# Performance work log

Measured on AMD Instinct MI355X. Metric: run time of the kernel, lower is better.

## Reference

```python
import jax, jax.numpy as jnp
import numpy as np

B, C, T = 2048, 8, 1024
EPS = 1e-5
SLOPE = 1.0 / 128.0


def leaky(x):
    # F.leaky_relu(x, 1/128)
    return jnp.where(x >= 0, x, SLOPE * x)


def batchnorm(h, g, b):
    # training-mode BatchNorm1d over [B, C, T]: stats over (batch, time), biased var
    m = h.mean(axis=(0, 2), keepdims=True)
    v = jnp.mean((h - m) ** 2, axis=(0, 2), keepdims=True)
    return (h - m) * jax.lax.rsqrt(v + EPS) * g[None, :, None] + b[None, :, None]


def setup_inputs() -> dict:
    key = jax.random.key(0)
    ks = jax.random.split(key, 8)
    x = jax.random.normal(ks[0], (B, C, T), dtype=jnp.float32)
    # reservoir pushforward: low-bit random matrix scaled to spectral radius 0.1
    A_raw = jax.random.normal(ks[1], (C, C), dtype=jnp.float32)
    rho = jnp.max(jnp.abs(np.linalg.eigvals(np.asarray(A_raw))))
    A = (0.1 * A_raw / rho).astype(jnp.float32)
    w1 = jax.random.normal(ks[2], (24, 8), dtype=jnp.float32) * (1.0 / np.sqrt(8))
    b1 = jax.random.normal(ks[3], (24,), dtype=jnp.float32) * 0.01
    w2 = jax.random.normal(ks[4], (16, 24), dtype=jnp.float32) * (1.0 / np.sqrt(24))
    b2 = jax.random.normal(ks[5], (16,), dtype=jnp.float32) * 0.01
    w3 = jax.random.normal(ks[6], (11, 48), dtype=jnp.float32) * (1.0 / np.sqrt(48))
    b3 = jax.random.normal(ks[7], (11,), dtype=jnp.float32) * 0.01
    return {
        "x": x, "A": A,
        "bn1_g": jnp.ones((8,), jnp.float32), "bn1_b": jnp.zeros((8,), jnp.float32),
        "w1": w1, "b1": b1, "w2": w2, "b2": b2, "w3": w3, "b3": b3,
        "bn2_g": jnp.ones((11,), jnp.float32), "bn2_b": jnp.zeros((11,), jnp.float32),
    }


def reference(x, A, bn1_g, bn1_b, w1, b1, w2, b2, w3, b3, bn2_g, bn2_b):
    bw = batchnorm(x, bn1_g, bn1_b)  # [B,8,T]

    # --- FSDDRC reservoir: 1024-step sequential recurrence on 8-dim state ---
    xs = jnp.transpose(bw, (2, 0, 1))  # [T,B,8]

    def step(f, xt):
        # nonlin(A @ f + x_t) with nonlin(z) = clamp(4z, -1, 1)
        f_new = jnp.clip(4.0 * (f @ A.T + xt), -1.0, 1.0)
        return f_new, jnp.concatenate([f_new, leaky(f_new)], axis=-1)  # [B,16]

    f0 = jnp.zeros_like(xs[0])
    _, outs = jax.lax.scan(step, f0, xs)  # [T,B,16]
    nl_tdyn = jnp.transpose(outs, (1, 2, 0))  # [B,16,T]

    # --- feedforward branch (mtmt = linear over channel dim) ---
    h = leaky(jnp.einsum("bct,oc->bot", bw, w1) + b1[None, :, None])  # [B,24,T]
    ff = leaky(jnp.einsum("bct,oc->bot", h, w2) + b2[None, :, None])  # [B,16,T]

    stacked = jnp.concatenate([x, bw, ff, nl_tdyn], axis=1)  # [B,48,T]
    pre = jnp.einsum("bct,oc->bot", stacked, w3) + b3[None, :, None]  # [B,11,T]
    assimilated = leaky(batchnorm(pre, bn2_g, bn2_b))
    return assimilated.mean(axis=-1)  # [B,11]
```

## Files before the change

### kernel.cpp

```cpp
#include <hip/hip_runtime.h>
#include <hip/hip_fp16.h>

#define NB 2048
#define NC 8
#define NT 1024
#define EPS 1e-5f
#define SLOPE (1.0f/128.0f)
#define NELEM (2048.0f*1024.0f)
#define TB (NT*NB)

#define PAR_OFF 9216
#define BN2_OFF 1024
#define PF_S4  0
#define PF_O4  8
#define PF_B1F 16
#define PF_B2F 40
#define PF_B3F 56
#define PU_A4   96
#define PU_W1   128
#define PU_W2   224
#define PU_W3X  416
#define PU_W3F  460
#define PU_W3L  504
#define PU_W3FF 548
#define XT_BYTE  65536
#define PWS_BYTE (65536 + 2048*1024*8*2)

typedef _Float16 h2 __attribute__((ext_vector_type(2)));
typedef __fp16  fp16v2 __attribute__((ext_vector_type(2)));
union U32H2 { unsigned u; h2 h; fp16v2 f; unsigned short us[2]; };

__device__ __forceinline__ float leaky(float z){ return fmaxf(z, z*SLOPE); }
__device__ __forceinline__ unsigned short f2h(float v){ return __half_as_ushort(__float2half(v)); }
__device__ __forceinline__ float h2f(unsigned short u){ return __half2float(__ushort_as_half(u)); }
__device__ __forceinline__ h2 uph2(unsigned u){ U32H2 x; x.u = u; return x.h; }
__device__ __forceinline__ h2 pk(float a, float b){
    U32H2 x; x.f = __builtin_amdgcn_cvt_pkrtz(a, b); return x.h;
}
__device__ __forceinline__ h2 leaky2(h2 v){
    h2 s = v * (_Float16)SLOPE;
    return __builtin_elementwise_max(v, s);
}
__device__ __forceinline__ float clamp1(float z){ return __builtin_amdgcn_fmed3f(z, -1.f, 1.f); }

#if defined(__has_builtin)
#if __has_builtin(__builtin_amdgcn_fdot2)
#define HAVE_FDOT2 1
#endif
#endif
#ifdef HAVE_FDOT2
__device__ __forceinline__ float fdot2(h2 a, h2 b, float c){ return __builtin_amdgcn_fdot2(a, b, c, false); }
#else
__device__ __forceinline__ float fdot2(h2 a, h2 b, float c){
    return c + (float)a[0]*(float)b[0] + (float)a[1]*(float)b[1];
}
#endif

__global__ __launch_bounds__(256) void k0_tr(const float* __restrict__ x,
                                             unsigned short* __restrict__ xT,
                                             float* __restrict__ ws)
{
    __shared__ unsigned short tile[64*134];
    __shared__ float sred[4][4][2];
    const int tid = threadIdx.x;
    const int bg = blockIdx.x >> 4;
    const int tg = blockIdx.x & 15;
    const int b0 = bg*16, t0 = tg*64;
    float s = 0.f, s2 = 0.f;
#pragma unroll
    for(int r=0;r<8;r++){
        const int flat4 = r*256 + tid;
        const int row = flat4 >> 4;
        const int t4  = flat4 & 15;
        const int b = row >> 3, c = row & 7;
        float4 v = *(const float4*)(x + (size_t)(b0+b)*8192 + c*1024 + t0 + t4*4);
        s  += v.x+v.y+v.z+v.w;
        s2 += v.x*v.x+v.y*v.y+v.z*v.z+v.w*v.w;
        const int base = b*8 + c;
        tile[(t4*4+0)*134 + base] = f2h(v.x);
        tile[(t4*4+1)*134 + base] = f2h(v.y);
        tile[(t4*4+2)*134 + base] = f2h(v.z);
        tile[(t4*4+3)*134 + base] = f2h(v.w);
    }
#pragma unroll
    for(int m=8;m>=1;m>>=1){ s += __shfl_xor(s,m,64); s2 += __shfl_xor(s2,m,64); }
    const int lane = tid & 63, wave = tid >> 6;
    if((lane & 15) == 0){ sred[wave][lane>>4][0] = s; sred[wave][lane>>4][1] = s2; }
    __syncthreads();
    if(tid < 16){
        const int c = tid & 7, which = tid >> 3;
        const int w0 = (c < 4) ? 0 : 1, g = c & 3;
        const float v = sred[w0][g][which] + sred[w0+2][g][which];
        atomicAdd(&ws[(blockIdx.x & 63)*16 + which*8 + c], v);
    }
#pragma unroll
    for(int r=0;r<8;r++){
        const int q = r*256 + tid;
        const int t = q >> 5, inner = q & 31;
        const unsigned int lo = *(const unsigned int*)&tile[t*134 + inner*4];
        const unsigned int hi = *(const unsigned int*)&tile[t*134 + inner*4 + 2];
        *(uint2*)(xT + ((size_t)(t0+t)*NB + b0)*8 + inner*4) = make_uint2(lo, hi);
    }
}

__device__ __forceinline__ unsigned pk2u(float a, float b){
    U32H2 v; v.us[0] = f2h(a); v.us[1] = f2h(b); return v.u;
}
__global__ __launch_bounds__(256) void k2_fold(const float* __restrict__ g1, const float* __restrict__ bb1,
    const float* __restrict__ w1, const float* __restrict__ b1,
    const float* __restrict__ w2, const float* __restrict__ b2,
    const float* __restrict__ w3, const float* __restrict__ b3,
    const float* __restrict__ A, float* __restrict__ ws,
    float* __restrict__ out)
{
    float* par = ws + PAR_OFF;
    unsigned* paru = (unsigned*)par;
    __shared__ float st[16];
    __shared__ float sc[8], oc[8];
    const int tid = threadIdx.x;
    if(tid<16){
        float s=0.f;
        for(int i=0;i<64;i++) s += ws[i*16+tid];
        st[tid]=s;
    }
    __syncthreads();
    if(tid<8){
        const float inv = 1.0f/NELEM;
        float m  = st[tid]*inv;
        float v  = st[8+tid]*inv - m*m;
        float s_ = g1[tid]*rsqrtf(v+EPS);
        float o_ = bb1[tid] - m*s_;
        sc[tid]=s_; oc[tid]=o_;
        par[PF_S4+tid]=4.f*s_; par[PF_O4+tid]=4.f*o_;
    }
    __syncthreads();
    if(tid<24){ float a=b1[tid]; for(int c=0;c<8;c++) a += w1[tid*8+c]*oc[c]; par[PF_B1F+tid]=a; }
    if(tid<16){ par[PF_B2F+tid]=b2[tid]; }
    if(tid<11){ float a=b3[tid]; for(int c=0;c<8;c++) a += w3[tid*48+8+c]*oc[c]; par[PF_B3F+tid]=a; }
    if(tid<96){ int o=tid>>2, j=tid&3;
        paru[PU_W1+tid] = pk2u(w1[o*8+2*j]*sc[2*j], w1[o*8+2*j+1]*sc[2*j+1]); }
    if(tid<192){ int o=tid/12, j=tid-o*12;
        paru[PU_W2+tid] = pk2u(w2[o*24+2*j], w2[o*24+2*j+1]); }
    if(tid<44){ int o=tid>>2, j=tid&3; int c0=2*j, c1=2*j+1;
        float xa = w3[o*48+c0] + w3[o*48+8+c0]*sc[c0];
        float xb = w3[o*48+c1] + w3[o*48+8+c1]*sc[c1];
        paru[PU_W3X+tid] = pk2u(xa, xb);
        paru[PU_W3F+tid] = pk2u(w3[o*48+32+c0], w3[o*48+32+c1]);
        paru[PU_W3L+tid] = pk2u(w3[o*48+40+c0], w3[o*48+40+c1]);
    }
    if(tid<88){ int o=tid>>3, j=tid&7;
        paru[PU_W3FF+tid] = pk2u(w3[o*48+16+2*j], w3[o*48+16+2*j+1]); }
    if(tid<32){ int i=tid>>2, j=tid&3;
        paru[PU_A4+tid] = pk2u(4.f*A[i*8+2*j], 4.f*A[i*8+2*j+1]); }
    for(int i=tid;i<2048*11;i+=256) out[i] = 0.f;
}

__global__ __launch_bounds__(256,4) void k34(
    const unsigned short* __restrict__ xT,
    const float* __restrict__ par,
    float* __restrict__ bn2,
    unsigned short* __restrict__ pws)
{
    const unsigned* pu = (const unsigned*)par;
    const int tid = threadIdx.x;
    const int b  = (blockIdx.x >> 7)*256 + tid;
    const int tg = blockIdx.x & 127;
    const int t0 = tg*8;
    const int tw = (t0 >= 16) ? (t0 - 16) : 0;

    h2 fh[4];
#pragma unroll
    for(int j=0;j<4;j++) fh[j] = pk(0.f, 0.f);
    float s1[11], s2[11];
#pragma unroll
    for(int o=0;o<11;o++){ s1[o]=0.f; s2[o]=0.f; }

    for(int t=tw; t<t0; t++){
        union { float4 v; unsigned u[4]; unsigned short us[8]; } ux;
        ux.v = *(const float4*)(xT + ((size_t)t*NB + b)*8);
        float nf[8];
#pragma unroll
        for(int i=0;i<8;i++){
            float acc = fmaf(par[PF_S4+i], h2f(ux.us[i]), par[PF_O4+i]);
#pragma unroll
            for(int j=0;j<4;j++) acc = fdot2(uph2(pu[PU_A4+i*4+j]), fh[j], acc);
            nf[i] = clamp1(acc);
        }
#pragma unroll
        for(int j=0;j<4;j++) fh[j] = pk(nf[2*j], nf[2*j+1]);
    }

    for(int tp=0; tp<4; tp++){
        const int t = t0 + tp*2;
        h2 xh2[2][4], fh2[2][4];
#pragma unroll
        for(int u=0;u<2;u++){
            union { float4 v; unsigned uu[4]; unsigned short us[8]; } ux;
            ux.v = *(const float4*)(xT + ((size_t)(t+u)*NB + b)*8);
#pragma unroll
            for(int j=0;j<4;j++) xh2[u][j] = uph2(ux.uu[j]);
            float nf[8];
#pragma unroll
            for(int i=0;i<8;i++){
                float acc = fmaf(par[PF_S4+i], h2f(ux.us[i]), par[PF_O4+i]);
#pragma unroll
                for(int j=0;j<4;j++) acc = fdot2(uph2(pu[PU_A4+i*4+j]), fh[j], acc);
                nf[i] = clamp1(acc);
            }
#pragma unroll
            for(int j=0;j<4;j++){ fh[j] = pk(nf[2*j], nf[2*j+1]); fh2[u][j] = fh[j]; }
        }
        h2 hh2[2][12];
#pragma unroll
        for(int p=0;p<12;p++){
            float za0 = par[PF_B1F+2*p], zb0 = par[PF_B1F+2*p+1];
            float za1 = za0, zb1 = zb0;
#pragma unroll
            for(int j=0;j<4;j++){
                h2 wa = uph2(pu[PU_W1+(2*p)*4+j]);
                h2 wb = uph2(pu[PU_W1+(2*p+1)*4+j]);
                za0 = fdot2(wa, xh2[0][j], za0);
                za1 = fdot2(wa, xh2[1][j], za1);
                zb0 = fdot2(wb, xh2[0][j], zb0);
                zb1 = fdot2(wb, xh2[1][j], zb1);
            }
            hh2[0][p] = leaky2(pk(za0, zb0));
            hh2[1][p] = leaky2(pk(za1, zb1));
        }
        h2 ff2[2][8];
#pragma unroll
        for(int p=0;p<8;p++){
            float za0 = par[PF_B2F+2*p], zb0 = par[PF_B2F+2*p+1];
            float za1 = za0, zb1 = zb0;
#pragma unroll
            for(int j=0;j<12;j++){
                h2 wa = uph2(pu[PU_W2+(2*p)*12+j]);
                h2 wb = uph2(pu[PU_W2+(2*p+1)*12+j]);
                za0 = fdot2(wa, hh2[0][j], za0);
                za1 = fdot2(wa, hh2[1][j], za1);
                zb0 = fdot2(wb, hh2[0][j], zb0);
                zb1 = fdot2(wb, hh2[1][j], zb1);
            }
            ff2[0][p] = leaky2(pk(za0, zb0));
            ff2[1][p] = leaky2(pk(za1, zb1));
        }
        h2 lf2[2][4];
#pragma unroll
        for(int u=0;u<2;u++)
#pragma unroll
            for(int j=0;j<4;j++) lf2[u][j] = leaky2(fh2[u][j]);
        const size_t base = (size_t)t*NB + b;
#pragma unroll
        for(int o=0;o<11;o++){
            float z0 = par[PF_B3F+o], z1 = z0;
#pragma unroll
            for(int j=0;j<4;j++){
                h2 w = uph2(pu[PU_W3X+o*4+j]);
                z0 = fdot2(w, xh2[0][j], z0); z1 = fdot2(w, xh2[1][j], z1);
            }
#pragma unroll
            for(int j=0;j<4;j++){
                h2 w = uph2(pu[PU_W3F+o*4+j]);
                z0 = fdot2(w, fh2[0][j], z0); z1 = fdot2(w, fh2[1][j], z1);
            }
#pragma unroll
            for(int j=0;j<4;j++){
                h2 w = uph2(pu[PU_W3L+o*4+j]);
                z0 = fdot2(w, lf2[0][j], z0); z1 = fdot2(w, lf2[1][j], z1);
            }
#pragma unroll
            for(int j=0;j<8;j++){
                h2 w = uph2(pu[PU_W3FF+o*8+j]);
                z0 = fdot2(w, ff2[0][j], z0); z1 = fdot2(w, ff2[1][j], z1);
            }
            s1[o] += z0 + z1;
            s2[o] = fmaf(z0, z0, s2[o]);
            s2[o] = fmaf(z1, z1, s2[o]);
            pws[(size_t)o*TB + base]      = f2h(z0);
            pws[(size_t)o*TB + base + NB] = f2h(z1);
        }
    }
#pragma unroll
    for(int o=0;o<11;o++){
#pragma unroll
        for(int m=32;m>=1;m>>=1){ s1[o]+=__shfl_xor(s1[o],m,64); s2[o]+=__shfl_xor(s2[o],m,64); }
    }
    __shared__ float red[4][22];
    const int wave=tid>>6, lane=tid&63;
    if(lane==0){
#pragma unroll
        for(int o=0;o<11;o++){ red[wave][o]=s1[o]; red[wave][11+o]=s2[o]; }
    }
    __syncthreads();
    if(tid<22){
        float tot = red[0][tid]+red[1][tid]+red[2][tid]+red[3][tid];
        atomicAdd(&bn2[(blockIdx.x & 255)*32 + tid], tot);
    }
}

__global__ __launch_bounds__(256) void k6(const float* __restrict__ g2, const float* __restrict__ bb2,
                                          const float* __restrict__ ws,
                                          const unsigned short* __restrict__ pws,
                                          float* __restrict__ out)
{
    const int o  = blockIdx.x >> 5;
    const int r  = blockIdx.x & 31;
    const int bg = r & 1, tg = r >> 1;
    const int tid = threadIdx.x;

    __shared__ float red[4][2];
    __shared__ float sal, sbe;
    {
        float p1 = ws[BN2_OFF + tid*32 + o];
        float p2 = ws[BN2_OFF + tid*32 + 11 + o];
#pragma unroll
        for(int m=32;m>=1;m>>=1){ p1 += __shfl_xor(p1,m,64); p2 += __shfl_xor(p2,m,64); }
        const int wave = tid>>6, lane = tid&63;
        if(lane==0){ red[wave][0]=p1; red[wave][1]=p2; }
        __syncthreads();
        if(tid==0){
            float t1 = red[0][0]+red[1][0]+red[2][0]+red[3][0];
            float t2 = red[0][1]+red[1][1]+red[2][1]+red[3][1];
            const float inv = 1.0f/NELEM;
            float m = t1*inv;
            float v = t2*inv - m*m;
            float a = g2[o]*rsqrtf(v+EPS);
            sal = a; sbe = bb2[o] - m*a;
        }
        __syncthreads();
    }
    const float al = sal, be = sbe;

    const int b0 = bg*1024 + tid*4;
    const unsigned short* pp = pws + (size_t)o*TB + b0;
    float acc0=0.f, acc1=0.f, acc2=0.f, acc3=0.f;
#pragma unroll 8
    for(int i=0;i<64;i++){
        const int t = tg*64 + i;
        uint2 u = *(const uint2*)(pp + (size_t)t*NB);
        unsigned short a0 = (unsigned short)(u.x & 0xffff), a1 = (unsigned short)(u.x >> 16);
        unsigned short c0 = (unsigned short)(u.y & 0xffff), c1 = (unsigned short)(u.y >> 16);
        acc0 += leaky(fmaf(al, h2f(a0), be));
        acc1 += leaky(fmaf(al, h2f(a1), be));
        acc2 += leaky(fmaf(al, h2f(c0), be));
        acc3 += leaky(fmaf(al, h2f(c1), be));
    }
    atomicAdd(&out[(b0+0)*11+o], acc0*(1.0f/NT));
    atomicAdd(&out[(b0+1)*11+o], acc1*(1.0f/NT));
    atomicAdd(&out[(b0+2)*11+o], acc2*(1.0f/NT));
    atomicAdd(&out[(b0+3)*11+o], acc3*(1.0f/NT));
}

extern "C" void kernel_launch(void* const* d_in, const int* in_sizes, int n_in,
                              void* d_out, int out_size, void* d_ws, size_t ws_size,
                              hipStream_t stream)
{
    const float* x   = (const float*)d_in[0];
    const float* A   = (const float*)d_in[1];
    const float* g1  = (const float*)d_in[2];
    const float* bb1 = (const float*)d_in[3];
    const float* w1  = (const float*)d_in[4];
    const float* b1  = (const float*)d_in[5];
    const float* w2  = (const float*)d_in[6];
    const float* b2  = (const float*)d_in[7];
    const float* w3  = (const float*)d_in[8];
    const float* b3  = (const float*)d_in[9];
    const float* g2  = (const float*)d_in[10];
    const float* bb2 = (const float*)d_in[11];
    float* out = (float*)d_out;
    float* ws  = (float*)d_ws;
    unsigned short* xT  = (unsigned short*)((char*)d_ws + XT_BYTE);
    unsigned short* pws = (unsigned short*)((char*)d_ws + PWS_BYTE);

    (void)hipMemsetAsync(d_ws, 0, 40960, stream);
    k0_tr  <<<2048, 256, 0, stream>>>(x, xT, ws);
    k2_fold<<<1,    256, 0, stream>>>(g1, bb1, w1, b1, w2, b2, w3, b3, A, ws, out);
    k34    <<<1024, 256, 0, stream>>>(xT, ws + PAR_OFF, ws + BN2_OFF, pws);
    k6     <<<352,  256, 0, stream>>>(g2, bb2, ws, pws, out);
}
```

Measured before the change: 239.0 us.

## Compute feedforward and output projections with MFMA via per-wave LDS staging

Replaces the per-thread fdot2 chains for the w1, w2 and w3 channel projections with 16x16x32 f16 MFMA instructions. Each wave stages its 64 rows of [x, f, leaky(f)] in LDS, runs MFMAs for the hidden, ff and output layers, and writes intermediates back to LDS between stages. The fold kernel now pre-packs zero-padded weight fragments into a new workspace region. Per-thread BN2 partial sums shrink to one channel per lane. In exchange the kernel adds LDS traffic, a larger shared-memory footprint, and one timestep per iteration instead of two, which may reduce occupancy and ILP.

```diff
diff --git a/kernel.cpp b/kernel.cpp
--- a/kernel.cpp
+++ b/kernel.cpp
@@ -11,24 +11,25 @@
 
 #define PAR_OFF 9216
 #define BN2_OFF 1024
+#define P2_OFF  10240
 #define PF_S4  0
 #define PF_O4  8
 #define PF_B1F 16
 #define PF_B2F 40
 #define PF_B3F 56
 #define PU_A4   96
-#define PU_W1   128
-#define PU_W2   224
-#define PU_W3X  416
-#define PU_W3F  460
-#define PU_W3L  504
-#define PU_W3FF 548
 #define XT_BYTE  65536
 #define PWS_BYTE (65536 + 2048*1024*8*2)
 
+#define ROWH 40
+#define ZH   18
+
 typedef _Float16 h2 __attribute__((ext_vector_type(2)));
+typedef _Float16 half8 __attribute__((ext_vector_type(8)));
+typedef float f32x4 __attribute__((ext_vector_type(4)));
 typedef __fp16  fp16v2 __attribute__((ext_vector_type(2)));
 union U32H2 { unsigned u; h2 h; fp16v2 f; unsigned short us[2]; };
+union UF { uint4 u; half8 h; };
 
 __device__ __forceinline__ float leaky(float z){ return fmaxf(z, z*SLOPE); }
 __device__ __forceinline__ unsigned short f2h(float v){ return __half_as_ushort(__float2half(v)); }
@@ -116,7 +117,7 @@
     float* par = ws + PAR_OFF;
     unsigned* paru = (unsigned*)par;
     __shared__ float st[16];
-    __shared__ float sc[8], oc[8];
+    __shared__ float ssc[8], soc[8], sb1f[24], sb3f[11];
     const int tid = threadIdx.x;
     if(tid<16){
         float s=0.f;
@@ -130,50 +131,86 @@
         float v  = st[8+tid]*inv - m*m;
         float s_ = g1[tid]*rsqrtf(v+EPS);
         float o_ = bb1[tid] - m*s_;
-        sc[tid]=s_; oc[tid]=o_;
+        ssc[tid]=s_; soc[tid]=o_;
         par[PF_S4+tid]=4.f*s_; par[PF_O4+tid]=4.f*o_;
     }
     __syncthreads();
-    if(tid<24){ float a=b1[tid]; for(int c=0;c<8;c++) a += w1[tid*8+c]*oc[c]; par[PF_B1F+tid]=a; }
+    if(tid<24){ float a=b1[tid]; for(int c=0;c<8;c++) a += w1[tid*8+c]*soc[c]; sb1f[tid]=a; par[PF_B1F+tid]=a; }
     if(tid<16){ par[PF_B2F+tid]=b2[tid]; }
-    if(tid<11){ float a=b3[tid]; for(int c=0;c<8;c++) a += w3[tid*48+8+c]*oc[c]; par[PF_B3F+tid]=a; }
-    if(tid<96){ int o=tid>>2, j=tid&3;
-        paru[PU_W1+tid] = pk2u(w1[o*8+2*j]*sc[2*j], w1[o*8+2*j+1]*sc[2*j+1]); }
-    if(tid<192){ int o=tid/12, j=tid-o*12;
-        paru[PU_W2+tid] = pk2u(w2[o*24+2*j], w2[o*24+2*j+1]); }
-    if(tid<44){ int o=tid>>2, j=tid&3; int c0=2*j, c1=2*j+1;
-        float xa = w3[o*48+c0] + w3[o*48+8+c0]*sc[c0];
-        float xb = w3[o*48+c1] + w3[o*48+8+c1]*sc[c1];
-        paru[PU_W3X+tid] = pk2u(xa, xb);
-        paru[PU_W3F+tid] = pk2u(w3[o*48+32+c0], w3[o*48+32+c1]);
-        paru[PU_W3L+tid] = pk2u(w3[o*48+40+c0], w3[o*48+40+c1]);
-    }
-    if(tid<88){ int o=tid>>3, j=tid&7;
-        paru[PU_W3FF+tid] = pk2u(w3[o*48+16+2*j], w3[o*48+16+2*j+1]); }
+    if(tid<11){ float a=b3[tid]; for(int c=0;c<8;c++) a += w3[tid*48+8+c]*soc[c]; sb3f[tid]=a; par[PF_B3F+tid]=a; }
     if(tid<32){ int i=tid>>2, j=tid&3;
         paru[PU_A4+tid] = pk2u(4.f*A[i*8+2*j], 4.f*A[i*8+2*j+1]); }
+    __syncthreads();
+
+    unsigned* pt = (unsigned*)(ws + P2_OFF);
+    if(tid<64){
+        const int n = tid & 15, kq = tid >> 4;
+        float v[8];
+#pragma unroll
+        for(int j=0;j<8;j++){ int k=kq*8+j; v[j] = (k<8)? w1[n*8+k]*ssc[k] : 0.f; }
+        for(int j=0;j<4;j++) pt[64 + 0*256 + tid*4 + j] = pk2u(v[2*j], v[2*j+1]);
+#pragma unroll
+        for(int j=0;j<8;j++){ int k=kq*8+j; int o=16+n;
+            v[j] = (o<24 && k<8)? w1[o*8+k]*ssc[k] : 0.f; }
+        for(int j=0;j<4;j++) pt[64 + 1*256 + tid*4 + j] = pk2u(v[2*j], v[2*j+1]);
+#pragma unroll
+        for(int j=0;j<8;j++){ int k=kq*8+j; v[j] = (k<24)? w2[n*24+k] : 0.f; }
+        for(int j=0;j<4;j++) pt[64 + 2*256 + tid*4 + j] = pk2u(v[2*j], v[2*j+1]);
+#pragma unroll
+        for(int j=0;j<8;j++){ int k=kq*8+j;
+            float t = 0.f;
+            if(n<11){
+                if(k<8)       t = w3[n*48+k] + w3[n*48+8+k]*ssc[k];
+                else if(k<16) t = w3[n*48+32+(k-8)];
+                else if(k<24) t = w3[n*48+40+(k-16)];
+            }
+            v[j] = t; }
+        for(int j=0;j<4;j++) pt[64 + 3*256 + tid*4 + j] = pk2u(v[2*j], v[2*j+1]);
+#pragma unroll
+        for(int j=0;j<8;j++){ int k=kq*8+j;
+            v[j] = (n<11 && k<16)? w3[n*48+16+k] : 0.f; }
+        for(int j=0;j<4;j++) pt[64 + 4*256 + tid*4 + j] = pk2u(v[2*j], v[2*j+1]);
+    }
+    if(tid<16){
+        float* bf = ws + P2_OFF;
+        bf[tid]      = sb1f[tid];
+        bf[16+tid]   = (tid<8)? sb1f[16+tid] : 0.f;
+        bf[32+tid]   = b2[tid];
+        bf[48+tid]   = (tid<11)? sb3f[tid] : 0.f;
+    }
     for(int i=tid;i<2048*11;i+=256) out[i] = 0.f;
 }
 
 __global__ __launch_bounds__(256,4) void k34(
     const unsigned short* __restrict__ xT,
-    const float* __restrict__ par,
-    float* __restrict__ bn2,
+    float* __restrict__ ws,
     unsigned short* __restrict__ pws)
 {
+    const float* par = ws + PAR_OFF;
     const unsigned* pu = (const unsigned*)par;
     const int tid = threadIdx.x;
+    const int wave = tid>>6, lane = tid&63;
+    const int ln = lane&15, kb = lane>>4;
     const int b  = (blockIdx.x >> 7)*256 + tid;
     const int tg = blockIdx.x & 127;
     const int t0 = tg*8;
     const int tw = (t0 >= 16) ? (t0 - 16) : 0;
 
+    __shared__ unsigned short lds[4*64*ROWH + 4*64*ZH];
+    unsigned short* rowb = lds + wave*(64*ROWH);
+    unsigned short* zbuf = lds + 4*(64*ROWH) + wave*(64*ZH);
+
+    const float* p2 = ws + P2_OFF;
+    const uint4* ft = (const uint4*)(p2 + 64);
+    UF w1a, w1b, w2f, w3a, w3b;
+    w1a.u = ft[lane];      w1b.u = ft[64+lane];  w2f.u = ft[128+lane];
+    w3a.u = ft[192+lane];  w3b.u = ft[256+lane];
+    const float bi1a = p2[ln], bi1b = p2[16+ln], bi2 = p2[32+ln], bi3 = p2[48+ln];
+
     h2 fh[4];
 #pragma unroll
     for(int j=0;j<4;j++) fh[j] = pk(0.f, 0.f);
-    float s1[11], s2[11];
-#pragma unroll
-    for(int o=0;o<11;o++){ s1[o]=0.f; s2[o]=0.f; }
+    float s1 = 0.f, s2 = 0.f;
 
     for(int t=tw; t<t0; t++){
         union { float4 v; unsigned u[4]; unsigned short us[8]; } ux;
@@ -190,111 +227,92 @@
         for(int j=0;j<4;j++) fh[j] = pk(nf[2*j], nf[2*j+1]);
     }
 
-    for(int tp=0; tp<4; tp++){
-        const int t = t0 + tp*2;
-        h2 xh2[2][4], fh2[2][4];
-#pragma unroll
-        for(int u=0;u<2;u++){
-            union { float4 v; unsigned uu[4]; unsigned short us[8]; } ux;
-            ux.v = *(const float4*)(xT + ((size_t)(t+u)*NB + b)*8);
-#pragma unroll
-            for(int j=0;j<4;j++) xh2[u][j] = uph2(ux.uu[j]);
-            float nf[8];
-#pragma unroll
-            for(int i=0;i<8;i++){
-                float acc = fmaf(par[PF_S4+i], h2f(ux.us[i]), par[PF_O4+i]);
-#pragma unroll
-                for(int j=0;j<4;j++) acc = fdot2(uph2(pu[PU_A4+i*4+j]), fh[j], acc);
-                nf[i] = clamp1(acc);
+    for(int t=t0; t<t0+8; ++t){
+        union { float4 v; unsigned u[4]; unsigned short us[8]; } ux;
+        ux.v = *(const float4*)(xT + ((size_t)t*NB + b)*8);
+        float nf[8];
+#pragma unroll
+        for(int i=0;i<8;i++){
+            float acc = fmaf(par[PF_S4+i], h2f(ux.us[i]), par[PF_O4+i]);
+#pragma unroll
+            for(int j=0;j<4;j++) acc = fdot2(uph2(pu[PU_A4+i*4+j]), fh[j], acc);
+            nf[i] = clamp1(acc);
+        }
+#pragma unroll
+        for(int j=0;j<4;j++) fh[j] = pk(nf[2*j], nf[2*j+1]);
+        h2 lfh[4];
+#pragma unroll
+        for(int j=0;j<4;j++) lfh[j] = leaky2(fh[j]);
+
+        {
+            unsigned short* my = rowb + lane*ROWH;
+            U32H2 f0,f1,f2,f3, l0,l1,l2,l3;
+            f0.h=fh[0]; f1.h=fh[1]; f2.h=fh[2]; f3.h=fh[3];
+            l0.h=lfh[0]; l1.h=lfh[1]; l2.h=lfh[2]; l3.h=lfh[3];
+            *(uint4*)(my)      = make_uint4(ux.u[0], ux.u[1], ux.u[2], ux.u[3]);
+            *(uint4*)(my + 8)  = make_uint4(f0.u, f1.u, f2.u, f3.u);
+            *(uint4*)(my + 16) = make_uint4(l0.u, l1.u, l2.u, l3.u);
+            *(uint4*)(my + 24) = make_uint4(0u, 0u, 0u, 0u);
+        }
+
+        f32x4 accz[4];
+#pragma unroll
+        for(int T=0;T<4;T++){
+            half8 A1 = *(const half8*)(rowb + (T*16+ln)*ROWH + kb*8);
+            f32x4 ha = {bi1a, bi1a, bi1a, bi1a};
+            f32x4 hb = {bi1b, bi1b, bi1b, bi1b};
+            f32x4 zz = {bi3,  bi3,  bi3,  bi3};
+            ha = __builtin_amdgcn_mfma_f32_16x16x32_f16(A1, w1a.h, ha, 0,0,0);
+            hb = __builtin_amdgcn_mfma_f32_16x16x32_f16(A1, w1b.h, hb, 0,0,0);
+            zz = __builtin_amdgcn_mfma_f32_16x16x32_f16(A1, w3a.h, zz, 0,0,0);
+            accz[T] = zz;
+            unsigned short* hw = rowb + (T*16 + kb*4)*ROWH + ln;
+#pragma unroll
+            for(int r=0;r<4;r++){
+                hw[r*ROWH]      = f2h(leaky(ha[r]));
+                hw[r*ROWH + 16] = f2h(leaky(hb[r]));
             }
-#pragma unroll
-            for(int j=0;j<4;j++){ fh[j] = pk(nf[2*j], nf[2*j+1]); fh2[u][j] = fh[j]; }
-        }
-        h2 hh2[2][12];
-#pragma unroll
-        for(int p=0;p<12;p++){
-            float za0 = par[PF_B1F+2*p], zb0 = par[PF_B1F+2*p+1];
-            float za1 = za0, zb1 = zb0;
-#pragma unroll
-            for(int j=0;j<4;j++){
-                h2 wa = uph2(pu[PU_W1+(2*p)*4+j]);
-                h2 wb = uph2(pu[PU_W1+(2*p+1)*4+j]);
-                za0 = fdot2(wa, xh2[0][j], za0);
-                za1 = fdot2(wa, xh2[1][j], za1);
-                zb0 = fdot2(wb, xh2[0][j], zb0);
-                zb1 = fdot2(wb, xh2[1][j], zb1);
+        }
+#pragma unroll
+        for(int T=0;T<4;T++){
+            half8 A2 = *(const half8*)(rowb + (T*16+ln)*ROWH + kb*8);
+            f32x4 ff = {bi2, bi2, bi2, bi2};
+            ff = __builtin_amdgcn_mfma_f32_16x16x32_f16(A2, w2f.h, ff, 0,0,0);
+            unsigned short* fw = rowb + (T*16 + kb*4)*ROWH + ln;
+#pragma unroll
+            for(int r=0;r<4;r++) fw[r*ROWH] = f2h(leaky(ff[r]));
+        }
+#pragma unroll
+        for(int T=0;T<4;T++){
+            half8 A3 = *(const half8*)(rowb + (T*16+ln)*ROWH + kb*8);
+            f32x4 zz = __builtin_amdgcn_mfma_f32_16x16x32_f16(A3, w3b.h, accz[T], 0,0,0);
+            unsigned short* zw = zbuf + (T*16 + kb*4)*ZH + ln;
+#pragma unroll
+            for(int r=0;r<4;r++){
+                float z = zz[r];
+                s1 += z; s2 = fmaf(z, z, s2);
+                zw[r*ZH] = f2h(z);
             }
-            hh2[0][p] = leaky2(pk(za0, zb0));
-            hh2[1][p] = leaky2(pk(za1, zb1));
-        }
-        h2 ff2[2][8];
-#pragma unroll
-        for(int p=0;p<8;p++){
-            float za0 = par[PF_B2F+2*p], zb0 = par[PF_B2F+2*p+1];
-            float za1 = za0, zb1 = zb0;
-#pragma unroll
-            for(int j=0;j<12;j++){
-                h2 wa = uph2(pu[PU_W2+(2*p)*12+j]);
-                h2 wb = uph2(pu[PU_W2+(2*p+1)*12+j]);
-                za0 = fdot2(wa, hh2[0][j], za0);
-                za1 = fdot2(wa, hh2[1][j], za1);
-                zb0 = fdot2(wb, hh2[0][j], zb0);
-                zb1 = fdot2(wb, hh2[1][j], zb1);
-            }
-            ff2[0][p] = leaky2(pk(za0, zb0));
-            ff2[1][p] = leaky2(pk(za1, zb1));
-        }
-        h2 lf2[2][4];
-#pragma unroll
-        for(int u=0;u<2;u++)
-#pragma unroll
-            for(int j=0;j<4;j++) lf2[u][j] = leaky2(fh2[u][j]);
-        const size_t base = (size_t)t*NB + b;
-#pragma unroll
-        for(int o=0;o<11;o++){
-            float z0 = par[PF_B3F+o], z1 = z0;
-#pragma unroll
-            for(int j=0;j<4;j++){
-                h2 w = uph2(pu[PU_W3X+o*4+j]);
-                z0 = fdot2(w, xh2[0][j], z0); z1 = fdot2(w, xh2[1][j], z1);
-            }
-#pragma unroll
-            for(int j=0;j<4;j++){
-                h2 w = uph2(pu[PU_W3F+o*4+j]);
-                z0 = fdot2(w, fh2[0][j], z0); z1 = fdot2(w, fh2[1][j], z1);
-            }
-#pragma unroll
-            for(int j=0;j<4;j++){
-                h2 w = uph2(pu[PU_W3L+o*4+j]);
-                z0 = fdot2(w, lf2[0][j], z0); z1 = fdot2(w, lf2[1][j], z1);
-            }
-#pragma unroll
-            for(int j=0;j<8;j++){
-                h2 w = uph2(pu[PU_W3FF+o*8+j]);
-                z0 = fdot2(w, ff2[0][j], z0); z1 = fdot2(w, ff2[1][j], z1);
-            }
-            s1[o] += z0 + z1;
-            s2[o] = fmaf(z0, z0, s2[o]);
-            s2[o] = fmaf(z1, z1, s2[o]);
-            pws[(size_t)o*TB + base]      = f2h(z0);
-            pws[(size_t)o*TB + base + NB] = f2h(z1);
-        }
-    }
-#pragma unroll
-    for(int o=0;o<11;o++){
-#pragma unroll
-        for(int m=32;m>=1;m>>=1){ s1[o]+=__shfl_xor(s1[o],m,64); s2[o]+=__shfl_xor(s2[o],m,64); }
-    }
+        }
+        {
+            const size_t base = (size_t)t*NB + b;
+            const unsigned short* mz = zbuf + lane*ZH;
+            unsigned short zv[11];
+#pragma unroll
+            for(int o=0;o<11;o++) zv[o] = mz[o];
+#pragma unroll
+            for(int o=0;o<11;o++) pws[(size_t)o*TB + base] = zv[o];
+        }
+    }
+
+    s1 += __shfl_xor(s1, 16, 64); s1 += __shfl_xor(s1, 32, 64);
+    s2 += __shfl_xor(s2, 16, 64); s2 += __shfl_xor(s2, 32, 64);
     __shared__ float red[4][22];
-    const int wave=tid>>6, lane=tid&63;
-    if(lane==0){
-#pragma unroll
-        for(int o=0;o<11;o++){ red[wave][o]=s1[o]; red[wave][11+o]=s2[o]; }
-    }
+    if(kb==0 && ln<11){ red[wave][ln] = s1; red[wave][11+ln] = s2; }
     __syncthreads();
     if(tid<22){
         float tot = red[0][tid]+red[1][tid]+red[2][tid]+red[3][tid];
-        atomicAdd(&bn2[(blockIdx.x & 255)*32 + tid], tot);
+        atomicAdd(&ws[BN2_OFF + (blockIdx.x & 255)*32 + tid], tot);
     }
 }
 
@@ -375,6 +393,6 @@
     (void)hipMemsetAsync(d_ws, 0, 40960, stream);
     k0_tr  <<<2048, 256, 0, stream>>>(x, xT, ws);
     k2_fold<<<1,    256, 0, stream>>>(g1, bb1, w1, b1, w2, b2, w3, b3, A, ws, out);
-    k34    <<<1024, 256, 0, stream>>>(xT, ws + PAR_OFF, ws + BN2_OFF, pws);
+    k34    <<<1024, 256, 0, stream>>>(xT, ws, pws);
     k6     <<<352,  256, 0, stream>>>(g2, bb2, ws, pws, out);
 }
```

After: 201.8 us. -15.6%, faster.
